# Performance work log

Measured on AMD Instinct MI355X. Metric: run time of the kernel, lower is better.

Reference implementation:

```python
import jax, jax.numpy as jnp
import numpy as np

DIM = 128      # transformer_dim = bottleneck_ch
NHEADS = 4
NEXP = 16
EHID = 256
WS = 8         # window_size
EPS = 1e-5     # LayerNorm eps


def setup_inputs() -> dict:
    key = jax.random.key(0)
    ks = jax.random.split(key, 6)
    B, H, W = 2, 128, 128
    N = H * W
    s = 0.02
    return {
        "x": jax.random.normal(ks[0], (B, N, DIM), jnp.float32),
        "ln1_g": jnp.ones((DIM,), jnp.float32),
        "ln1_b": jnp.zeros((DIM,), jnp.float32),
        "w_qkv": jax.random.normal(ks[1], (3 * DIM, DIM), jnp.float32) * s,
        "b_qkv": jnp.zeros((3 * DIM,), jnp.float32),
        "w_proj": jax.random.normal(ks[2], (DIM, DIM), jnp.float32) * s,
        "b_proj": jnp.zeros((DIM,), jnp.float32),
        "ln2_g": jnp.ones((DIM,), jnp.float32),
        "ln2_b": jnp.zeros((DIM,), jnp.float32),
        "gate_w": jax.random.normal(ks[3], (NEXP, DIM), jnp.float32) * s,
        "w1": jax.random.normal(ks[4], (NEXP, EHID, DIM), jnp.float32) * s,
        "b1": jnp.zeros((NEXP, EHID), jnp.float32),
        "w2": jax.random.normal(ks[5], (NEXP, DIM, EHID), jnp.float32) * s,
        "b2": jnp.zeros((NEXP, DIM), jnp.float32),
        "H": H,
        "W": W,
    }


def _ln(x, g, b):
    m = jnp.mean(x, axis=-1, keepdims=True)
    v = jnp.var(x, axis=-1, keepdims=True)
    return (x - m) * jax.lax.rsqrt(v + EPS) * g + b


def _win_attn(x, H, W, w_qkv, b_qkv, w_proj, b_proj):
    # x: (B, N, C); H,W divisible by WS (no padding branch needed)
    B, N, C = x.shape
    hd = C // NHEADS
    nH, nW = H // WS, W // WS
    # window partition: (B, N, C) -> (B*nH*nW, WS*WS, C)
    xw = x.reshape(B, nH, WS, nW, WS, C).transpose(0, 1, 3, 2, 4, 5)
    xw = xw.reshape(B * nH * nW, WS * WS, C)
    qkv = xw @ w_qkv.T + b_qkv
    q, k, v = jnp.split(qkv, 3, axis=-1)
    def heads(t):
        return t.reshape(-1, WS * WS, NHEADS, hd).transpose(0, 2, 1, 3)
    q, k, v = heads(q), heads(k), heads(v)
    scores = jnp.einsum('whqd,whkd->whqk', q, k) / jnp.sqrt(jnp.float32(hd))
    a = jax.nn.softmax(scores, axis=-1)
    o = jnp.einsum('whqk,whkd->whqd', a, v).transpose(0, 2, 1, 3)
    o = o.reshape(-1, WS * WS, C) @ w_proj.T + b_proj
    # window merge back to (B, N, C)
    o = o.reshape(B, nH, nW, WS, WS, C).transpose(0, 1, 3, 2, 4, 5)
    return o.reshape(B, N, C)


def _moe(x, gate_w, w1, b1, w2, b2):
    # top_k = 1 routing, eval mode (no noise / aux losses)
    B, N, C = x.shape
    f = x.reshape(-1, C)                      # (T, C)
    logits = f @ gate_w.T                     # (T, E)
    probs = jax.nn.softmax(logits, axis=-1)
    p = jnp.max(probs, axis=-1)               # top-1 prob
    idx = jnp.argmax(probs, axis=-1)          # top-1 expert id
    wgt = p / (p + 1e-8)                      # top_k_probs / (sum + eps)
    out = jnp.zeros_like(f)
    for e in range(NEXP):                     # small fixed expert loop
        h = jax.nn.gelu(f @ w1[e].T + b1[e], approximate=False)
        eo = h @ w2[e].T + b2[e]
        out = out + jnp.where((idx == e)[:, None], eo, 0.0)
    return (out * wgt[:, None]).reshape(B, N, C)


def reference(x, ln1_g, ln1_b, w_qkv, b_qkv, w_proj, b_proj,
              ln2_g, ln2_b, gate_w, w1, b1, w2, b2, H, W):
    x = x + _win_attn(_ln(x, ln1_g, ln1_b), H, W, w_qkv, b_qkv, w_proj, b_proj)
    x = x + _moe(_ln(x, ln2_g, ln2_b), gate_w, w1, b1, w2, b2)
    return x
```

## Files before the change

### kernel.cpp

```cpp
#include <hip/hip_runtime.h>
#include <math.h>

#define T_TOK 32768
#define DIM 128
#define NHEADS 4
#define HD 32
#define NEXP 16
#define EHID 256
#define NWIN 512
#define EPS 1e-5f
#define CPAD 16

typedef _Float16 f16x8 __attribute__((ext_vector_type(8)));
typedef _Float16 f16x4 __attribute__((ext_vector_type(4)));
typedef float f32x4v __attribute__((ext_vector_type(4)));

#define MFMA16(a, b, c) __builtin_amdgcn_mfma_f32_16x16x32_f16(a, b, c, 0, 0, 0)
#define LO_SCALE 4096.0f
#define LO_INV (1.0f / 4096.0f)

__device__ __forceinline__ int sw128(int r, int c) {
    return r * 128 + (((c >> 3) ^ (r & 7)) << 3) + (c & 7);
}
__device__ __forceinline__ int sw64(int r, int c) {
    return r * 64 + (((c >> 3) ^ (r & 7)) << 3) + (c & 7);
}
__device__ __forceinline__ int swht(int tok, int hid) {
    return tok * 256 + (((hid >> 3) ^ (tok & 7)) << 3) + (hid & 7);
}

__global__ __launch_bounds__(256) void k_cvt(
    const float* __restrict__ wqkv, const float* __restrict__ wproj,
    const float* __restrict__ w1, const float* __restrict__ w2,
    _Float16* __restrict__ wq_h, _Float16* __restrict__ wq_l,
    _Float16* __restrict__ wp_h, _Float16* __restrict__ wp_l,
    _Float16* __restrict__ w1h, _Float16* __restrict__ w2h,
    int* __restrict__ counts)
{
    int i = blockIdx.x * 256 + threadIdx.x;
    if (blockIdx.x == 0 && threadIdx.x < NEXP * CPAD) counts[threadIdx.x] = 0;
    {
        float4 a = ((const float4*)w1)[i];
        f16x4 h;
        h[0] = (_Float16)a.x; h[1] = (_Float16)a.y; h[2] = (_Float16)a.z; h[3] = (_Float16)a.w;
        *(f16x4*)(w1h + (size_t)i * 4) = h;
        float4 b = ((const float4*)w2)[i];
        f16x4 h2;
        h2[0] = (_Float16)b.x; h2[1] = (_Float16)b.y; h2[2] = (_Float16)b.z; h2[3] = (_Float16)b.w;
        *(f16x4*)(w2h + (size_t)i * 4) = h2;
    }
    if (i < 3 * DIM * DIM / 4) {
        float4 f = ((const float4*)wqkv)[i];
        float fv[4] = {f.x, f.y, f.z, f.w};
        f16x4 h, l;
        #pragma unroll
        for (int j = 0; j < 4; ++j) {
            _Float16 hh = (_Float16)fv[j];
            h[j] = hh;
            l[j] = (_Float16)((fv[j] - (float)hh) * LO_SCALE);
        }
        *(f16x4*)(wq_h + (size_t)i * 4) = h;
        *(f16x4*)(wq_l + (size_t)i * 4) = l;
    }
    if (i < DIM * DIM / 4) {
        float4 f = ((const float4*)wproj)[i];
        float fv[4] = {f.x, f.y, f.z, f.w};
        f16x4 h, l;
        #pragma unroll
        for (int j = 0; j < 4; ++j) {
            _Float16 hh = (_Float16)fv[j];
            h[j] = hh;
            l[j] = (_Float16)((fv[j] - (float)hh) * LO_SCALE);
        }
        *(f16x4*)(wp_h + (size_t)i * 4) = h;
        *(f16x4*)(wp_l + (size_t)i * 4) = l;
    }
}

__global__ __launch_bounds__(512) void k_attn(
    const float* __restrict__ x,
    const float* __restrict__ ln_g, const float* __restrict__ ln_b,
    const _Float16* __restrict__ wq_h, const _Float16* __restrict__ wq_l,
    const float* __restrict__ b_qkv,
    const _Float16* __restrict__ wp_h, const _Float16* __restrict__ wp_l,
    const float* __restrict__ b_proj,
    float* __restrict__ x2)
{
    __shared__ _Float16 xoh[64 * 128], xol[64 * 128];
    __shared__ _Float16 qh[64 * 128],  ql[64 * 128];
    __shared__ _Float16 kh[64 * 128],  kl[64 * 128];
    __shared__ _Float16 vth[128 * 64], vtl[128 * 64];

    int tid = threadIdx.x;
    int w = tid >> 6, lane = tid & 63;
    int l15 = lane & 15, lg = lane >> 4;
    int wid = blockIdx.x;
    int wb = wid >> 8, wrr = (wid >> 4) & 15, wcc = wid & 15;
    const size_t base = ((size_t)wb * 16384 + (size_t)wrr * 1024 + (size_t)wcc * 8) * DIM;

    {
        int tt = tid >> 3, sub = tid & 7;
        const float* xr = x + base + (size_t)(tt >> 3) * 16384 + (size_t)(tt & 7) * DIM + sub * 16;
        float v[16];
        float s = 0.f, sq = 0.f;
        #pragma unroll
        for (int j = 0; j < 4; ++j) {
            float4 t4 = *(const float4*)(xr + j * 4);
            v[4 * j] = t4.x; v[4 * j + 1] = t4.y; v[4 * j + 2] = t4.z; v[4 * j + 3] = t4.w;
            s += (t4.x + t4.y) + (t4.z + t4.w);
            sq = fmaf(t4.x, t4.x, fmaf(t4.y, t4.y, fmaf(t4.z, t4.z, fmaf(t4.w, t4.w, sq))));
        }
        s += __shfl_xor(s, 1); sq += __shfl_xor(sq, 1);
        s += __shfl_xor(s, 2); sq += __shfl_xor(sq, 2);
        s += __shfl_xor(s, 4); sq += __shfl_xor(sq, 4);
        float m = s * (1.f / DIM);
        float var = sq * (1.f / DIM) - m * m;
        float rs = rsqrtf(var + EPS);
        _Float16 hh[16], ll[16];
        #pragma unroll
        for (int j = 0; j < 16; ++j) {
            int k = sub * 16 + j;
            float a = (v[j] - m) * rs * ln_g[k] + ln_b[k];
            _Float16 h = (_Float16)a;
            hh[j] = h;
            ll[j] = (_Float16)((a - (float)h) * LO_SCALE);
        }
        *(f16x8*)&xoh[sw128(tt, sub * 16)]     = *(const f16x8*)&hh[0];
        *(f16x8*)&xoh[sw128(tt, sub * 16 + 8)] = *(const f16x8*)&hh[8];
        *(f16x8*)&xol[sw128(tt, sub * 16)]     = *(const f16x8*)&ll[0];
        *(f16x8*)&xol[sw128(tt, sub * 16 + 8)] = *(const f16x8*)&ll[8];
    }
    __syncthreads();

    #pragma unroll
    for (int ct = 0; ct < 3; ++ct) {
        int o = w * 48 + ct * 16 + l15;
        f16x8 bh[4], bl[4];
        #pragma unroll
        for (int ks = 0; ks < 4; ++ks) {
            size_t wo = (size_t)o * DIM + ks * 32 + lg * 8;
            bh[ks] = *(const f16x8*)(wq_h + wo);
            bl[ks] = *(const f16x8*)(wq_l + wo);
        }
        f32x4v am[4], ac[4];
        #pragma unroll
        for (int rt = 0; rt < 4; ++rt) { am[rt] = 0.0f; ac[rt] = 0.0f; }
        #pragma unroll
        for (int rt = 0; rt < 4; ++rt) {
            #pragma unroll
            for (int ks = 0; ks < 4; ++ks) {
                f16x8 ah = *(const f16x8*)&xoh[sw128(rt * 16 + l15, ks * 32 + lg * 8)];
                f16x8 al = *(const f16x8*)&xol[sw128(rt * 16 + l15, ks * 32 + lg * 8)];
                am[rt] = MFMA16(ah, bh[ks], am[rt]);
                ac[rt] = MFMA16(ah, bl[ks], ac[rt]);
                ac[rt] = MFMA16(al, bh[ks], ac[rt]);
            }
        }
        float bias = b_qkv[o];
        if (o < 256) {
            #pragma unroll
            for (int rt = 0; rt < 4; ++rt) {
                #pragma unroll
                for (int r = 0; r < 4; ++r) {
                    int row = rt * 16 + lg * 4 + r;
                    float val = am[rt][r] + ac[rt][r] * LO_INV + bias;
                    _Float16 h = (_Float16)val;
                    _Float16 lo = (_Float16)((val - (float)h) * LO_SCALE);
                    if (o < 128) { qh[sw128(row, o)] = h;       ql[sw128(row, o)] = lo; }
                    else         { kh[sw128(row, o - 128)] = h; kl[sw128(row, o - 128)] = lo; }
                }
            }
        } else {
            int d = o - 256;
            #pragma unroll
            for (int rt = 0; rt < 4; ++rt) {
                f16x4 vh4, vl4;
                #pragma unroll
                for (int r = 0; r < 4; ++r) {
                    float val = am[rt][r] + ac[rt][r] * LO_INV + bias;
                    _Float16 h = (_Float16)val;
                    vh4[r] = h;
                    vl4[r] = (_Float16)((val - (float)h) * LO_SCALE);
                }
                int tok0 = rt * 16 + lg * 4;
                *(f16x4*)&vth[sw64(d, tok0)] = vh4;
                *(f16x4*)&vtl[sw64(d, tok0)] = vl4;
            }
        }
    }
    __syncthreads();

    const float scale = 0.17677669529663687f;
    int h = w & 3;
    int qo = h * HD, rgb = (w >> 2) * 2;
    float preg[2][4][4];
    {
        f16x8 kbh[4], kbl[4];
        #pragma unroll
        for (int ct = 0; ct < 4; ++ct) {
            kbh[ct] = *(const f16x8*)&kh[sw128(ct * 16 + l15, qo + lg * 8)];
            kbl[ct] = *(const f16x8*)&kl[sw128(ct * 16 + l15, qo + lg * 8)];
        }
        #pragma unroll
        for (int t = 0; t < 2; ++t) {
            int rg = rgb + t;
            f16x8 qah = *(const f16x8*)&qh[sw128(rg * 16 + l15, qo + lg * 8)];
            f16x8 qal = *(const f16x8*)&ql[sw128(rg * 16 + l15, qo + lg * 8)];
            f32x4v sm[4], sc2[4];
            #pragma unroll
            for (int ct = 0; ct < 4; ++ct) {
                sm[ct] = 0.0f; sc2[ct] = 0.0f;
                sm[ct] = MFMA16(qah, kbh[ct], sm[ct]);
                sc2[ct] = MFMA16(qah, kbl[ct], sc2[ct]);
                sc2[ct] = MFMA16(qal, kbh[ct], sc2[ct]);
            }
            #pragma unroll
            for (int r = 0; r < 4; ++r) {
                float v0 = (sm[0][r] + sc2[0][r] * LO_INV) * scale;
                float v1 = (sm[1][r] + sc2[1][r] * LO_INV) * scale;
                float v2 = (sm[2][r] + sc2[2][r] * LO_INV) * scale;
                float v3 = (sm[3][r] + sc2[3][r] * LO_INV) * scale;
                float mx = fmaxf(fmaxf(v0, v1), fmaxf(v2, v3));
                mx = fmaxf(mx, __shfl_xor(mx, 1));
                mx = fmaxf(mx, __shfl_xor(mx, 2));
                mx = fmaxf(mx, __shfl_xor(mx, 4));
                mx = fmaxf(mx, __shfl_xor(mx, 8));
                float e0 = expf(v0 - mx), e1 = expf(v1 - mx), e2 = expf(v2 - mx), e3 = expf(v3 - mx);
                float ss = (e0 + e1) + (e2 + e3);
                ss += __shfl_xor(ss, 1); ss += __shfl_xor(ss, 2);
                ss += __shfl_xor(ss, 4); ss += __shfl_xor(ss, 8);
                float inv = 1.f / ss;
                preg[t][0][r] = e0 * inv;
                preg[t][1][r] = e1 * inv;
                preg[t][2][r] = e2 * inv;
                preg[t][3][r] = e3 * inv;
            }
        }
    }
    __syncthreads();

    {
        _Float16* dsth = (h < 2) ? qh : kh;
        _Float16* dstl = (h < 2) ? ql : kl;
        int pb = (h & 1) * 4096;
        #pragma unroll
        for (int t = 0; t < 2; ++t) {
            int rg = rgb + t;
            #pragma unroll
            for (int ct = 0; ct < 4; ++ct) {
                #pragma unroll
                for (int r = 0; r < 4; ++r) {
                    float p = preg[t][ct][r];
                    int row = rg * 16 + lg * 4 + r, col = ct * 16 + l15;
                    _Float16 hh = (_Float16)p;
                    dsth[pb + sw64(row, col)] = hh;
                    dstl[pb + sw64(row, col)] = (_Float16)((p - (float)hh) * LO_SCALE);
                }
            }
        }
    }

    {
        const _Float16* psh = (h < 2) ? qh : kh;
        const _Float16* psl = (h < 2) ? ql : kl;
        int pb = (h & 1) * 4096;
        f16x8 vbh[2][2], vbl[2][2];
        #pragma unroll
        for (int ks = 0; ks < 2; ++ks)
            #pragma unroll
            for (int ct = 0; ct < 2; ++ct) {
                vbh[ks][ct] = *(const f16x8*)&vth[sw64(qo + ct * 16 + l15, ks * 32 + lg * 8)];
                vbl[ks][ct] = *(const f16x8*)&vtl[sw64(qo + ct * 16 + l15, ks * 32 + lg * 8)];
            }
        #pragma unroll
        for (int t = 0; t < 2; ++t) {
            int rg = rgb + t;
            f32x4v om[2], oc[2];
            om[0] = 0.0f; om[1] = 0.0f; oc[0] = 0.0f; oc[1] = 0.0f;
            #pragma unroll
            for (int ks = 0; ks < 2; ++ks) {
                f16x8 pah = *(const f16x8*)&psh[pb + sw64(rg * 16 + l15, ks * 32 + lg * 8)];
                f16x8 pal = *(const f16x8*)&psl[pb + sw64(rg * 16 + l15, ks * 32 + lg * 8)];
                #pragma unroll
                for (int ct = 0; ct < 2; ++ct) {
                    om[ct] = MFMA16(pah, vbh[ks][ct], om[ct]);
                    oc[ct] = MFMA16(pah, vbl[ks][ct], oc[ct]);
                    oc[ct] = MFMA16(pal, vbh[ks][ct], oc[ct]);
                }
            }
            #pragma unroll
            for (int ct = 0; ct < 2; ++ct) {
                #pragma unroll
                for (int r = 0; r < 4; ++r) {
                    float val = om[ct][r] + oc[ct][r] * LO_INV;
                    int row = rg * 16 + lg * 4 + r, col = qo + ct * 16 + l15;
                    _Float16 hh = (_Float16)val;
                    xoh[sw128(row, col)] = hh;
                    xol[sw128(row, col)] = (_Float16)((val - (float)hh) * LO_SCALE);
                }
            }
        }
    }
    __syncthreads();

    {
        int rt = w & 3, cb = (w >> 2) * 64;
        f32x4v pm[4], pc[4];
        #pragma unroll
        for (int ct = 0; ct < 4; ++ct) { pm[ct] = 0.0f; pc[ct] = 0.0f; }
        #pragma unroll
        for (int ks = 0; ks < 4; ++ks) {
            f16x8 ah = *(const f16x8*)&xoh[sw128(rt * 16 + l15, ks * 32 + lg * 8)];
            f16x8 al = *(const f16x8*)&xol[sw128(rt * 16 + l15, ks * 32 + lg * 8)];
            #pragma unroll
            for (int ct = 0; ct < 4; ++ct) {
                int c = cb + ct * 16 + l15;
                f16x8 bh = *(const f16x8*)(wp_h + (size_t)c * DIM + ks * 32 + lg * 8);
                f16x8 bl = *(const f16x8*)(wp_l + (size_t)c * DIM + ks * 32 + lg * 8);
                pm[ct] = MFMA16(ah, bh, pm[ct]);
                pc[ct] = MFMA16(ah, bl, pc[ct]);
                pc[ct] = MFMA16(al, bh, pc[ct]);
            }
        }
        #pragma unroll
        for (int ct = 0; ct < 4; ++ct) {
            int c = cb + ct * 16 + l15;
            float bp = b_proj[c];
            #pragma unroll
            for (int r = 0; r < 4; ++r) {
                int q = rt * 16 + lg * 4 + r;
                size_t go = base + (size_t)(q >> 3) * 16384 + (size_t)(q & 7) * DIM + c;
                x2[go] = x[go] + (pm[ct][r] + pc[ct][r] * LO_INV + bp);
            }
        }
    }
}

__global__ __launch_bounds__(256) void k_ln2_gate(
    const float* __restrict__ x2, const float* __restrict__ g, const float* __restrict__ b,
    const float* __restrict__ gw, _Float16* __restrict__ y2,
    float* __restrict__ wgt, int* __restrict__ perm, int* __restrict__ counts)
{
    __shared__ float yt[64][129];
    __shared__ float lgs[64][17];
    int tid = threadIdx.x;
    size_t t0 = (size_t)blockIdx.x * 64;

    {
        int tt = tid >> 2, sub = tid & 3;
        const float* xr = x2 + (t0 + tt) * DIM + sub * 32;
        float v[32];
        float s = 0.f, sq = 0.f;
        #pragma unroll
        for (int j = 0; j < 8; ++j) {
            float4 t4 = *(const float4*)(xr + j * 4);
            v[4 * j] = t4.x; v[4 * j + 1] = t4.y; v[4 * j + 2] = t4.z; v[4 * j + 3] = t4.w;
            s += (t4.x + t4.y) + (t4.z + t4.w);
            sq = fmaf(t4.x, t4.x, fmaf(t4.y, t4.y, fmaf(t4.z, t4.z, fmaf(t4.w, t4.w, sq))));
        }
        s += __shfl_xor(s, 1); sq += __shfl_xor(sq, 1);
        s += __shfl_xor(s, 2); sq += __shfl_xor(sq, 2);
        float m = s * (1.f / DIM);
        float var = sq * (1.f / DIM) - m * m;
        float rs = rsqrtf(var + EPS);
        _Float16 hh[32];
        #pragma unroll
        for (int j = 0; j < 32; ++j) {
            int k = sub * 32 + j;
            float a = (v[j] - m) * rs * g[k] + b[k];
            yt[tt][k] = a;
            hh[j] = (_Float16)a;
        }
        #pragma unroll
        for (int j = 0; j < 4; ++j)
            *(f16x8*)(y2 + (t0 + tt) * DIM + sub * 32 + j * 8) = *(const f16x8*)&hh[j * 8];
    }
    __syncthreads();

    {
        int tt = tid & 63, eg = tid >> 6;
        const float* g0 = gw + (eg * 4 + 0) * DIM;
        const float* g1 = gw + (eg * 4 + 1) * DIM;
        const float* g2 = gw + (eg * 4 + 2) * DIM;
        const float* g3 = gw + (eg * 4 + 3) * DIM;
        float a0 = 0.f, a1 = 0.f, a2 = 0.f, a3 = 0.f;
        #pragma unroll 8
        for (int k = 0; k < DIM; ++k) {
            float yv = yt[tt][k];
            a0 = fmaf(yv, g0[k], a0);
            a1 = fmaf(yv, g1[k], a1);
            a2 = fmaf(yv, g2[k], a2);
            a3 = fmaf(yv, g3[k], a3);
        }
        lgs[tt][eg * 4 + 0] = a0;
        lgs[tt][eg * 4 + 1] = a1;
        lgs[tt][eg * 4 + 2] = a2;
        lgs[tt][eg * 4 + 3] = a3;
    }
    __syncthreads();

    if (tid < 64) {
        float mx = -1e30f; int am = 0;
        #pragma unroll
        for (int e = 0; e < NEXP; ++e) {
            float v = lgs[tid][e];
            if (v > mx) { mx = v; am = e; }
        }
        float ss = 0.f;
        #pragma unroll
        for (int e = 0; e < NEXP; ++e) ss += expf(lgs[tid][e] - mx);
        float p = 1.f / ss;
        wgt[t0 + tid] = p / (p + 1e-8f);

        int myrank = 0, mycnt = 0;
        #pragma unroll
        for (int e = 0; e < NEXP; ++e) {
            unsigned long long mask = __ballot(am == e);
            if (am == e) myrank = (int)__popcll(mask & ((1ull << tid) - 1));
            if (tid == e) mycnt = (int)__popcll(mask);
        }
        int base = 0;
        if (tid < NEXP) base = atomicAdd(&counts[tid * CPAD], mycnt);
        base = __shfl(base, am);
        perm[(size_t)am * T_TOK + base + myrank] = (int)(t0 + tid);
    }
}

__global__ __launch_bounds__(256, 3) void k_expert(
    const _Float16* __restrict__ y2, const float* __restrict__ x2,
    const _Float16* __restrict__ w1h, const float* __restrict__ b1,
    const _Float16* __restrict__ w2h, const float* __restrict__ b2,
    const int* __restrict__ perm, const int* __restrict__ counts,
    const float* __restrict__ wgt, float* __restrict__ out)
{
    __shared__ _Float16 yt[64 * 128];
    __shared__ _Float16 ht[64 * 256];
    __shared__ int rows[64];

    int bflat = blockIdx.x;
    int e = -1, tile = 0, acc0 = 0;
    #pragma unroll
    for (int ee = 0; ee < NEXP; ++ee) {
        int t = (counts[ee * CPAD] + 63) >> 6;
        if (e < 0 && bflat < acc0 + t) { e = ee; tile = bflat - acc0; }
        acc0 += t;
    }
    if (e < 0) return;
    int cnt = counts[e * CPAD];
    int row0 = tile << 6;
    int nr = min(64, cnt - row0);
    int tid = threadIdx.x, wv = tid >> 6, lane = tid & 63;
    int l15 = lane & 15, lg = lane >> 4;

    if (tid < 64) rows[tid] = (tid < nr) ? perm[(size_t)e * T_TOK + row0 + tid] : 0;
    __syncthreads();
    f16x8 vz = (_Float16)0.0f;
    for (int i = tid; i < 1024; i += 256) {
        int tt = i >> 4, k = (i & 15) * 8;
        f16x8 val = vz;
        if (tt < nr) val = *(const f16x8*)(y2 + (size_t)rows[tt] * DIM + k);
        *(f16x8*)&yt[sw128(tt, k)] = val;
    }
    __syncthreads();

    {
        f16x8 yb[4][4];
        #pragma unroll
        for (int ct = 0; ct < 4; ++ct)
            #pragma unroll
            for (int ks = 0; ks < 4; ++ks)
                yb[ct][ks] = *(const f16x8*)&yt[sw128(ct * 16 + l15, ks * 32 + lg * 8)];
        #pragma unroll
        for (int rt = 0; rt < 4; ++rt) {
            int hid_row = wv * 64 + rt * 16 + l15;
            f16x8 a1[4];
            #pragma unroll
            for (int ks = 0; ks < 4; ++ks)
                a1[ks] = *(const f16x8*)(w1h + ((size_t)e * EHID + hid_row) * DIM + ks * 32 + lg * 8);
            f32x4v acc[4];
            #pragma unroll
            for (int ct = 0; ct < 4; ++ct) acc[ct] = 0.0f;
            #pragma unroll
            for (int ct = 0; ct < 4; ++ct)
                #pragma unroll
                for (int ks = 0; ks < 4; ++ks)
                    acc[ct] = MFMA16(a1[ks], yb[ct][ks], acc[ct]);
            int hid0 = wv * 64 + rt * 16 + lg * 4;
            float4 bb4 = *(const float4*)(b1 + e * EHID + hid0);
            float bbv[4] = {bb4.x, bb4.y, bb4.z, bb4.w};
            #pragma unroll
            for (int ct = 0; ct < 4; ++ct) {
                f16x4 hv;
                #pragma unroll
                for (int r = 0; r < 4; ++r) {
                    float a = acc[ct][r] + bbv[r];
                    float gl = 0.5f * a * (1.f + erff(a * 0.70710678118654752f));
                    hv[r] = (_Float16)gl;
                }
                int tok = ct * 16 + l15;
                *(f16x4*)&ht[swht(tok, hid0)] = hv;
            }
        }
    }
    __syncthreads();

    {
        f16x8 wb[2][8];
        #pragma unroll
        for (int ct = 0; ct < 2; ++ct) {
            int c = wv * 32 + ct * 16 + l15;
            #pragma unroll
            for (int ks = 0; ks < 8; ++ks)
                wb[ct][ks] = *(const f16x8*)(w2h + ((size_t)e * DIM + c) * EHID + ks * 32 + lg * 8);
        }
        #pragma unroll
        for (int rt = 0; rt < 4; ++rt) {
            f16x8 af[8];
            #pragma unroll
            for (int ks = 0; ks < 8; ++ks)
                af[ks] = *(const f16x8*)&ht[swht(rt * 16 + l15, ks * 32 + lg * 8)];
            f32x4v acc2[2];
            acc2[0] = 0.0f; acc2[1] = 0.0f;
            #pragma unroll
            for (int ks = 0; ks < 8; ++ks)
                #pragma unroll
                for (int ct = 0; ct < 2; ++ct)
                    acc2[ct] = MFMA16(af[ks], wb[ct][ks], acc2[ct]);
            #pragma unroll
            for (int ct = 0; ct < 2; ++ct) {
                int c = wv * 32 + ct * 16 + l15;
                float bb = b2[e * DIM + c];
                #pragma unroll
                for (int r = 0; r < 4; ++r) {
                    int tt = rt * 16 + lg * 4 + r;
                    if (tt < nr) {
                        int gtok = rows[tt];
                        size_t go = (size_t)gtok * DIM + c;
                        out[go] = x2[go] + wgt[gtok] * (acc2[ct][r] + bb);
                    }
                }
            }
        }
    }
}

extern "C" void kernel_launch(void* const* d_in, const int* in_sizes, int n_in,
                              void* d_out, int out_size, void* d_ws, size_t ws_size,
                              hipStream_t stream) {
    const float* x      = (const float*)d_in[0];
    const float* ln1_g  = (const float*)d_in[1];
    const float* ln1_b  = (const float*)d_in[2];
    const float* w_qkv  = (const float*)d_in[3];
    const float* b_qkv  = (const float*)d_in[4];
    const float* w_proj = (const float*)d_in[5];
    const float* b_proj = (const float*)d_in[6];
    const float* ln2_g  = (const float*)d_in[7];
    const float* ln2_b  = (const float*)d_in[8];
    const float* gate_w = (const float*)d_in[9];
    const float* w1     = (const float*)d_in[10];
    const float* b1     = (const float*)d_in[11];
    const float* w2     = (const float*)d_in[12];
    const float* b2     = (const float*)d_in[13];
    float* out = (float*)d_out;

    char* p = (char*)d_ws;
    float* x2 = (float*)p;                 p += (size_t)T_TOK * DIM * 4;
    _Float16* y2 = (_Float16*)p;           p += (size_t)T_TOK * DIM * 2;
    _Float16* wq_h = (_Float16*)p;         p += 3 * DIM * DIM * 2;
    _Float16* wq_l = (_Float16*)p;         p += 3 * DIM * DIM * 2;
    _Float16* wp_h = (_Float16*)p;         p += DIM * DIM * 2;
    _Float16* wp_l = (_Float16*)p;         p += DIM * DIM * 2;
    _Float16* w1h = (_Float16*)p;          p += NEXP * EHID * DIM * 2;
    _Float16* w2h = (_Float16*)p;          p += NEXP * EHID * DIM * 2;
    float* wgt = (float*)p;                p += T_TOK * 4;
    int* perm = (int*)p;                   p += (size_t)NEXP * T_TOK * 4;
    int* counts = (int*)p;                 p += NEXP * CPAD * 4;

    k_cvt<<<512, 256, 0, stream>>>(w_qkv, w_proj, w1, w2, wq_h, wq_l, wp_h, wp_l,
                                   w1h, w2h, counts);
    k_attn<<<NWIN, 512, 0, stream>>>(x, ln1_g, ln1_b, wq_h, wq_l, b_qkv,
                                     wp_h, wp_l, b_proj, x2);
    k_ln2_gate<<<T_TOK / 64, 256, 0, stream>>>(x2, ln2_g, ln2_b, gate_w, y2, wgt, perm, counts);
    k_expert<<<544, 256, 0, stream>>>(y2, x2, w1h, b1, w2h, b2, perm, counts, wgt, out);
}
```

Baseline: 116.2 us.

## Fuse LN2 and gating into attention kernel; preload weights into registers

Merges the separate LN2+gate+routing kernel into the tail of the windowed-attention kernel, using the projected output that is already on-chip (staged in LDS) instead of re-reading x2 from global memory. It also hoists the QKV and projection weight fragments and the residual x values into registers early, so their global loads overlap with other work. Register pressure rises sharply (many f16x8 arrays held live), which may cause spills or lower occupancy. Tokens are now processed in window order rather than contiguous order, which changes the permutation order fed to the expert kernel.

```diff
diff --git a/kernel.cpp b/kernel.cpp
--- a/kernel.cpp
+++ b/kernel.cpp
@@ -84,19 +84,58 @@
     const float* __restrict__ b_qkv,
     const _Float16* __restrict__ wp_h, const _Float16* __restrict__ wp_l,
     const float* __restrict__ b_proj,
-    float* __restrict__ x2)
+    const float* __restrict__ ln2_g, const float* __restrict__ ln2_b,
+    const float* __restrict__ gw,
+    float* __restrict__ x2, _Float16* __restrict__ y2,
+    float* __restrict__ wgt, int* __restrict__ perm, int* __restrict__ counts)
 {
-    __shared__ _Float16 xoh[64 * 128], xol[64 * 128];
-    __shared__ _Float16 qh[64 * 128],  ql[64 * 128];
-    __shared__ _Float16 kh[64 * 128],  kl[64 * 128];
-    __shared__ _Float16 vth[128 * 64], vtl[128 * 64];
+    __shared__ __align__(16) char smem[131072];
+    _Float16* xoh = (_Float16*)(smem);
+    _Float16* xol = (_Float16*)(smem + 16384);
+    _Float16* qh  = (_Float16*)(smem + 32768);
+    _Float16* ql  = (_Float16*)(smem + 49152);
+    _Float16* kh  = (_Float16*)(smem + 65536);
+    _Float16* kl  = (_Float16*)(smem + 81920);
+    _Float16* vth = (_Float16*)(smem + 98304);
+    _Float16* vtl = (_Float16*)(smem + 114688);
+    float* xf   = (float*)(smem + 32768);
+    float* ylds = (float*)(smem + 65792);
+    float* lgs  = (float*)(smem + 98816);
 
     int tid = threadIdx.x;
     int w = tid >> 6, lane = tid & 63;
     int l15 = lane & 15, lg = lane >> 4;
     int wid = blockIdx.x;
     int wb = wid >> 8, wrr = (wid >> 4) & 15, wcc = wid & 15;
-    const size_t base = ((size_t)wb * 16384 + (size_t)wrr * 1024 + (size_t)wcc * 8) * DIM;
+    const int tokbase = wb * 16384 + wrr * 1024 + wcc * 8;
+    const size_t base = (size_t)tokbase * DIM;
+
+    f16x8 qbh[3][4], qbl[3][4];
+    float qbias[3];
+    #pragma unroll
+    for (int ct = 0; ct < 3; ++ct) {
+        int o = w * 48 + ct * 16 + l15;
+        qbias[ct] = b_qkv[o];
+        #pragma unroll
+        for (int ks = 0; ks < 4; ++ks) {
+            size_t wo = (size_t)o * DIM + ks * 32 + lg * 8;
+            qbh[ct][ks] = *(const f16x8*)(wq_h + wo);
+            qbl[ct][ks] = *(const f16x8*)(wq_l + wo);
+        }
+    }
+    float xres[16];
+    {
+        int rt = w & 3, cb = (w >> 2) * 64;
+        #pragma unroll
+        for (int ct = 0; ct < 4; ++ct) {
+            int c = cb + ct * 16 + l15;
+            #pragma unroll
+            for (int r = 0; r < 4; ++r) {
+                int q = rt * 16 + lg * 4 + r;
+                xres[ct * 4 + r] = x[base + (size_t)(q >> 3) * 16384 + (size_t)(q & 7) * DIM + c];
+            }
+        }
+    }
 
     {
         int tt = tid >> 3, sub = tid & 7;
@@ -135,13 +174,6 @@
     #pragma unroll
     for (int ct = 0; ct < 3; ++ct) {
         int o = w * 48 + ct * 16 + l15;
-        f16x8 bh[4], bl[4];
-        #pragma unroll
-        for (int ks = 0; ks < 4; ++ks) {
-            size_t wo = (size_t)o * DIM + ks * 32 + lg * 8;
-            bh[ks] = *(const f16x8*)(wq_h + wo);
-            bl[ks] = *(const f16x8*)(wq_l + wo);
-        }
         f32x4v am[4], ac[4];
         #pragma unroll
         for (int rt = 0; rt < 4; ++rt) { am[rt] = 0.0f; ac[rt] = 0.0f; }
@@ -151,12 +183,12 @@
             for (int ks = 0; ks < 4; ++ks) {
                 f16x8 ah = *(const f16x8*)&xoh[sw128(rt * 16 + l15, ks * 32 + lg * 8)];
                 f16x8 al = *(const f16x8*)&xol[sw128(rt * 16 + l15, ks * 32 + lg * 8)];
-                am[rt] = MFMA16(ah, bh[ks], am[rt]);
-                ac[rt] = MFMA16(ah, bl[ks], ac[rt]);
-                ac[rt] = MFMA16(al, bh[ks], ac[rt]);
-            }
-        }
-        float bias = b_qkv[o];
+                am[rt] = MFMA16(ah, qbh[ct][ks], am[rt]);
+                ac[rt] = MFMA16(ah, qbl[ct][ks], ac[rt]);
+                ac[rt] = MFMA16(al, qbh[ct][ks], ac[rt]);
+            }
+        }
+        float bias = qbias[ct];
         if (o < 256) {
             #pragma unroll
             for (int rt = 0; rt < 4; ++rt) {
@@ -301,6 +333,22 @@
             }
         }
     }
+
+    f16x8 wpbh[4][4], wpbl[4][4];
+    float pbias[4];
+    {
+        int cb = (w >> 2) * 64;
+        #pragma unroll
+        for (int ct = 0; ct < 4; ++ct) {
+            int c = cb + ct * 16 + l15;
+            pbias[ct] = b_proj[c];
+            #pragma unroll
+            for (int ks = 0; ks < 4; ++ks) {
+                wpbh[ct][ks] = *(const f16x8*)(wp_h + (size_t)c * DIM + ks * 32 + lg * 8);
+                wpbl[ct][ks] = *(const f16x8*)(wp_l + (size_t)c * DIM + ks * 32 + lg * 8);
+            }
+        }
+    }
     __syncthreads();
 
     {
@@ -314,88 +362,71 @@
             f16x8 al = *(const f16x8*)&xol[sw128(rt * 16 + l15, ks * 32 + lg * 8)];
             #pragma unroll
             for (int ct = 0; ct < 4; ++ct) {
-                int c = cb + ct * 16 + l15;
-                f16x8 bh = *(const f16x8*)(wp_h + (size_t)c * DIM + ks * 32 + lg * 8);
-                f16x8 bl = *(const f16x8*)(wp_l + (size_t)c * DIM + ks * 32 + lg * 8);
-                pm[ct] = MFMA16(ah, bh, pm[ct]);
-                pc[ct] = MFMA16(ah, bl, pc[ct]);
-                pc[ct] = MFMA16(al, bh, pc[ct]);
+                pm[ct] = MFMA16(ah, wpbh[ct][ks], pm[ct]);
+                pc[ct] = MFMA16(ah, wpbl[ct][ks], pc[ct]);
+                pc[ct] = MFMA16(al, wpbh[ct][ks], pc[ct]);
             }
         }
         #pragma unroll
         for (int ct = 0; ct < 4; ++ct) {
             int c = cb + ct * 16 + l15;
-            float bp = b_proj[c];
             #pragma unroll
             for (int r = 0; r < 4; ++r) {
                 int q = rt * 16 + lg * 4 + r;
+                float val = xres[ct * 4 + r] + (pm[ct][r] + pc[ct][r] * LO_INV + pbias[ct]);
                 size_t go = base + (size_t)(q >> 3) * 16384 + (size_t)(q & 7) * DIM + c;
-                x2[go] = x[go] + (pm[ct][r] + pc[ct][r] * LO_INV + bp);
-            }
-        }
-    }
-}
-
-__global__ __launch_bounds__(256) void k_ln2_gate(
-    const float* __restrict__ x2, const float* __restrict__ g, const float* __restrict__ b,
-    const float* __restrict__ gw, _Float16* __restrict__ y2,
-    float* __restrict__ wgt, int* __restrict__ perm, int* __restrict__ counts)
-{
-    __shared__ float yt[64][129];
-    __shared__ float lgs[64][17];
-    int tid = threadIdx.x;
-    size_t t0 = (size_t)blockIdx.x * 64;
-
-    {
-        int tt = tid >> 2, sub = tid & 3;
-        const float* xr = x2 + (t0 + tt) * DIM + sub * 32;
-        float v[32];
+                x2[go] = val;
+                xf[q * 129 + c] = val;
+            }
+        }
+    }
+    __syncthreads();
+
+    {
+        int tt = tid >> 3, sub = tid & 7;
+        const float* xr = xf + tt * 129 + sub * 16;
+        float v[16];
         float s = 0.f, sq = 0.f;
         #pragma unroll
-        for (int j = 0; j < 8; ++j) {
-            float4 t4 = *(const float4*)(xr + j * 4);
-            v[4 * j] = t4.x; v[4 * j + 1] = t4.y; v[4 * j + 2] = t4.z; v[4 * j + 3] = t4.w;
-            s += (t4.x + t4.y) + (t4.z + t4.w);
-            sq = fmaf(t4.x, t4.x, fmaf(t4.y, t4.y, fmaf(t4.z, t4.z, fmaf(t4.w, t4.w, sq))));
+        for (int j = 0; j < 16; ++j) {
+            float t = xr[j];
+            v[j] = t;
+            s += t;
+            sq = fmaf(t, t, sq);
         }
         s += __shfl_xor(s, 1); sq += __shfl_xor(sq, 1);
         s += __shfl_xor(s, 2); sq += __shfl_xor(sq, 2);
+        s += __shfl_xor(s, 4); sq += __shfl_xor(sq, 4);
         float m = s * (1.f / DIM);
         float var = sq * (1.f / DIM) - m * m;
         float rs = rsqrtf(var + EPS);
-        _Float16 hh[32];
-        #pragma unroll
-        for (int j = 0; j < 32; ++j) {
-            int k = sub * 32 + j;
-            float a = (v[j] - m) * rs * g[k] + b[k];
-            yt[tt][k] = a;
+        _Float16 hh[16];
+        #pragma unroll
+        for (int j = 0; j < 16; ++j) {
+            int k = sub * 16 + j;
+            float a = (v[j] - m) * rs * ln2_g[k] + ln2_b[k];
+            ylds[tt * 129 + k] = a;
             hh[j] = (_Float16)a;
         }
-        #pragma unroll
-        for (int j = 0; j < 4; ++j)
-            *(f16x8*)(y2 + (t0 + tt) * DIM + sub * 32 + j * 8) = *(const f16x8*)&hh[j * 8];
-    }
-    __syncthreads();
-
-    {
-        int tt = tid & 63, eg = tid >> 6;
-        const float* g0 = gw + (eg * 4 + 0) * DIM;
-        const float* g1 = gw + (eg * 4 + 1) * DIM;
-        const float* g2 = gw + (eg * 4 + 2) * DIM;
-        const float* g3 = gw + (eg * 4 + 3) * DIM;
-        float a0 = 0.f, a1 = 0.f, a2 = 0.f, a3 = 0.f;
+        int gtok = tokbase + (tt >> 3) * 128 + (tt & 7);
+        *(f16x8*)(y2 + (size_t)gtok * DIM + sub * 16)     = *(const f16x8*)&hh[0];
+        *(f16x8*)(y2 + (size_t)gtok * DIM + sub * 16 + 8) = *(const f16x8*)&hh[8];
+    }
+    __syncthreads();
+
+    {
+        int tk = lane, eg = w;
+        const float* g0 = gw + (eg * 2 + 0) * DIM;
+        const float* g1 = gw + (eg * 2 + 1) * DIM;
+        float a0 = 0.f, a1 = 0.f;
         #pragma unroll 8
         for (int k = 0; k < DIM; ++k) {
-            float yv = yt[tt][k];
+            float yv = ylds[tk * 129 + k];
             a0 = fmaf(yv, g0[k], a0);
             a1 = fmaf(yv, g1[k], a1);
-            a2 = fmaf(yv, g2[k], a2);
-            a3 = fmaf(yv, g3[k], a3);
-        }
-        lgs[tt][eg * 4 + 0] = a0;
-        lgs[tt][eg * 4 + 1] = a1;
-        lgs[tt][eg * 4 + 2] = a2;
-        lgs[tt][eg * 4 + 3] = a3;
+        }
+        lgs[tk * 20 + eg * 2]     = a0;
+        lgs[tk * 20 + eg * 2 + 1] = a1;
     }
     __syncthreads();
 
@@ -403,14 +434,15 @@
         float mx = -1e30f; int am = 0;
         #pragma unroll
         for (int e = 0; e < NEXP; ++e) {
-            float v = lgs[tid][e];
+            float v = lgs[tid * 20 + e];
             if (v > mx) { mx = v; am = e; }
         }
         float ss = 0.f;
         #pragma unroll
-        for (int e = 0; e < NEXP; ++e) ss += expf(lgs[tid][e] - mx);
+        for (int e = 0; e < NEXP; ++e) ss += expf(lgs[tid * 20 + e] - mx);
         float p = 1.f / ss;
-        wgt[t0 + tid] = p / (p + 1e-8f);
+        int gtok = tokbase + (tid >> 3) * 128 + (tid & 7);
+        wgt[gtok] = p / (p + 1e-8f);
 
         int myrank = 0, mycnt = 0;
         #pragma unroll
@@ -419,10 +451,10 @@
             if (am == e) myrank = (int)__popcll(mask & ((1ull << tid) - 1));
             if (tid == e) mycnt = (int)__popcll(mask);
         }
-        int base = 0;
-        if (tid < NEXP) base = atomicAdd(&counts[tid * CPAD], mycnt);
-        base = __shfl(base, am);
-        perm[(size_t)am * T_TOK + base + myrank] = (int)(t0 + tid);
+        int bky = 0;
+        if (tid < NEXP) bky = atomicAdd(&counts[tid * CPAD], mycnt);
+        bky = __shfl(bky, am);
+        perm[(size_t)am * T_TOK + bky + myrank] = gtok;
     }
 }
 
@@ -579,7 +611,7 @@
     k_cvt<<<512, 256, 0, stream>>>(w_qkv, w_proj, w1, w2, wq_h, wq_l, wp_h, wp_l,
                                    w1h, w2h, counts);
     k_attn<<<NWIN, 512, 0, stream>>>(x, ln1_g, ln1_b, wq_h, wq_l, b_qkv,
-                                     wp_h, wp_l, b_proj, x2);
-    k_ln2_gate<<<T_TOK / 64, 256, 0, stream>>>(x2, ln2_g, ln2_b, gate_w, y2, wgt, perm, counts);
+                                     wp_h, wp_l, b_proj, ln2_g, ln2_b, gate_w,
+                                     x2, y2, wgt, perm, counts);
     k_expert<<<544, 256, 0, stream>>>(y2, x2, w1h, b1, w2h, b2, perm, counts, wgt, out);
 }
```

Measured after the change: 113.1 us. -2.7%, faster.
